# Kernel optimization log

Hardware: AMD Instinct MI355X
Metric: run time of the kernel (lower is better)

## Reference

```python
import jax, jax.numpy as jnp
import numpy as np

H = 16          # num_heads
DH = 128        # head_dim
TILE = 128      # tile_size
TOPK = 8        # top_k_tiles
NEG = -1e10


def _rotate_half(x):
    half = x.shape[-1] // 2
    return jnp.concatenate([-x[..., half:], x[..., :half]], axis=-1)


def setup_inputs() -> dict:
    key = jax.random.key(0)
    B, S, D = 2, 2048, H * DH
    ks = jax.random.split(key, 5)
    x = jax.random.normal(ks[0], (B, S, D), dtype=jnp.float32)
    scale = 0.02
    wq = jax.random.normal(ks[1], (D, H * DH), dtype=jnp.float32) * scale
    wk = jax.random.normal(ks[2], (D, H * DH), dtype=jnp.float32) * scale
    wv = jax.random.normal(ks[3], (D, H * DH), dtype=jnp.float32) * scale
    wo = jax.random.normal(ks[4], (H * DH, D), dtype=jnp.float32) * scale
    # RoPE tables: freqs_cis.real / .imag, shape [S, head_dim//2]
    inv_freq = 1.0 / (10000.0 ** (np.arange(0, DH, 2, dtype=np.float32) / DH))
    angles = np.arange(S, dtype=np.float32)[:, None] * inv_freq[None, :]
    cos = jnp.asarray(np.cos(angles), dtype=jnp.float32)
    sin = jnp.asarray(np.sin(angles), dtype=jnp.float32)
    return {"x": x, "wq": wq, "wk": wk, "wv": wv, "wo": wo, "cos": cos, "sin": sin}


def reference(x, wq, wk, wv, wo, cos, sin):
    B, S, D = x.shape
    # QKV projections -> [B, H, S, Dh]
    q = (x @ wq).reshape(B, S, H, DH).transpose(0, 2, 1, 3)
    k = (x @ wk).reshape(B, S, H, DH).transpose(0, 2, 1, 3)
    v = (x @ wv).reshape(B, S, H, DH).transpose(0, 2, 1, 3)
    # RoPE (half-split / rotate_half form), in fp32 as in source
    cf = jnp.concatenate([cos, cos], axis=-1)[None, None].astype(jnp.float32)  # [1,1,S,Dh]
    sf = jnp.concatenate([sin, sin], axis=-1)[None, None].astype(jnp.float32)
    q = q.astype(jnp.float32)
    k = k.astype(jnp.float32)
    q = q * cf + _rotate_half(q) * sf
    k = k * cf + _rotate_half(k) * sf
    # Full causal logits [B,H,S,S] (short-seq branch: seq_len <= 8192)
    scale = 1.0 / jnp.sqrt(jnp.float32(DH))
    logits = jnp.einsum('bhqd,bhkd->bhqk', q, k) * scale
    causal = jnp.tril(jnp.ones((S, S), dtype=bool))
    logits = jnp.where(causal[None, None], logits, NEG)
    # Tile scoring: softmax over representative rows, tile max-pool, top-k tiles
    num_tiles = S // TILE
    rep_pos = jnp.arange(TILE - 1, S, TILE)           # last query of each tile
    rep_w = jax.nn.softmax(logits[:, :, rep_pos, :], axis=-1)  # [B,H,nt,S]
    tile_scores = jnp.max(rep_w.reshape(B, H, num_tiles, num_tiles, TILE), axis=-1)
    _, group_tile_indices = jax.lax.top_k(tile_scores, min(TOPK, num_tiles))  # [B,H,nt,topk]
    # Full causal attention (explicit path, same math as dot_product_attention is_causal)
    weights = jax.nn.softmax(logits, axis=-1)
    out = jnp.einsum('bhqk,bhkd->bhqd', weights, v)
    out = out.transpose(0, 2, 1, 3).reshape(B, S, H * DH)
    out = out @ wo
    return out, group_tile_indices
```

## Files before the change

### kernel.cpp

```cpp
#include <hip/hip_runtime.h>
#include <cstdint>
#include <cstddef>


#define S_LEN 2048
#define NH 16
#define DHD 128
#define DMODEL 2048
#define MROWS 4096
#define SCALE 0.08838834764831845f
#define SCALE_L2E (0.08838834764831845f * 1.4426950408889634f)
#define NEG10 -1e10f

typedef short short8 __attribute__((ext_vector_type(8)));
typedef __bf16 bf16x8 __attribute__((ext_vector_type(8)));
typedef float f32x4 __attribute__((ext_vector_type(4)));

#define MFMA16(a, b, c) __builtin_amdgcn_mfma_f32_16x16x32_bf16((a), (b), (c), 0, 0, 0)

__device__ __forceinline__ void gl16(const void* g, void* s) {
  __builtin_amdgcn_global_load_lds(
      (const __attribute__((address_space(1))) void*)g,
      (__attribute__((address_space(3))) void*)s, 16, 0, 0);
}

__device__ __forceinline__ unsigned short f2bf(float f) {
  unsigned u = __float_as_uint(f);
  return (unsigned short)((u + 0x7fffu + ((u >> 16) & 1u)) >> 16);
}
__device__ __forceinline__ float bf2f(unsigned short h) {
  return __uint_as_float(((unsigned)h) << 16);
}

__global__ __launch_bounds__(256) void k_split_x(const float* __restrict__ x,
                                                 unsigned short* __restrict__ xh,
                                                 unsigned short* __restrict__ xl, int n4) {
  int i = blockIdx.x * blockDim.x + threadIdx.x;
  for (; i < n4; i += gridDim.x * blockDim.x) {
    float4 v = ((const float4*)x)[i];
    float f[4] = {v.x, v.y, v.z, v.w};
    unsigned short hh[4], ll[4];
#pragma unroll
    for (int j = 0; j < 4; j++) {
      hh[j] = f2bf(f[j]);
      ll[j] = f2bf(f[j] - bf2f(hh[j]));
    }
    ((ushort4*)xh)[i] = make_ushort4(hh[0], hh[1], hh[2], hh[3]);
    ((ushort4*)xl)[i] = make_ushort4(ll[0], ll[1], ll[2], ll[3]);
  }
}

template <int LO>
__global__ __launch_bounds__(256) void k_transw(const float* __restrict__ w,
                                                unsigned short* __restrict__ th,
                                                unsigned short* __restrict__ tl) {
  int n = blockIdx.x * 256 + threadIdx.x;
  int r0 = blockIdx.y * 32;
  float vals[32];
#pragma unroll
  for (int j = 0; j < 32; j++) vals[j] = w[(size_t)(r0 + j) * DMODEL + n];
  unsigned short hs[32];
#pragma unroll
  for (int j = 0; j < 32; j++) hs[j] = f2bf(vals[j]);
  unsigned short* dsth = th + (size_t)n * DMODEL + r0;
#pragma unroll
  for (int c = 0; c < 4; c++) {
    short8 v;
#pragma unroll
    for (int j = 0; j < 8; j++) v[j] = (short)hs[c * 8 + j];
    *(short8*)(dsth + c * 8) = v;
  }
  if (LO) {
    unsigned short ls[32];
#pragma unroll
    for (int j = 0; j < 32; j++) ls[j] = f2bf(vals[j] - bf2f(hs[j]));
    unsigned short* dstl = tl + (size_t)n * DMODEL + r0;
#pragma unroll
    for (int c = 0; c < 4; c++) {
      short8 v;
#pragma unroll
      for (int j = 0; j < 8; j++) v[j] = (short)ls[c * 8 + j];
      *(short8*)(dstl + c * 8) = v;
    }
  }
}

template <int SPLIT, int EPI>
__global__ __launch_bounds__(256) void k_gemm(const unsigned short* __restrict__ A,
                                              const unsigned short* __restrict__ Al,
                                              const unsigned short* __restrict__ Bt,
                                              const unsigned short* __restrict__ Btl,
                                              void* __restrict__ outp) {
  constexpr int NSM = (SPLIT ? 4 : 2) * 4096;
  __shared__ unsigned short sm[NSM];
  unsigned short* sAh = sm;
  unsigned short* sAl = SPLIT ? (sm + 4096) : nullptr;
  unsigned short* sBh = sm + (SPLIT ? 8192 : 4096);
  unsigned short* sBl = SPLIT ? (sm + 12288) : nullptr;

  const int tid = threadIdx.x;
  const int l = tid & 63, w = tid >> 6;
  const int lr = l & 15, lk = l >> 4;
  const int rowBase = blockIdx.y * 128;
  const int colBase = blockIdx.x * 128;
  const int wr = (w >> 1) * 64, wc = (w & 1) * 64;

  f32x4 zero = {0.f, 0.f, 0.f, 0.f};
  f32x4 acc[4][4];
#pragma unroll
  for (int mi = 0; mi < 4; mi++)
#pragma unroll
    for (int ni = 0; ni < 4; ni++) acc[mi][ni] = zero;

  for (int kt = 0; kt < 64; ++kt) {
#pragma unroll
    for (int p = 0; p < 2; ++p) {
      int c = w * 128 + p * 64 + l;
      int row = c >> 2, sl = c & 3;
      int kbl = sl ^ ((row >> 1) & 3);
      size_t srca = (size_t)(rowBase + row) * DMODEL + kt * 32 + kbl * 8;
      gl16(A + srca, (char*)sAh + c * 16);
      if (SPLIT) gl16(Al + srca, (char*)sAl + c * 16);
      size_t srcb = (size_t)(colBase + row) * DMODEL + kt * 32 + kbl * 8;
      gl16(Bt + srcb, (char*)sBh + c * 16);
      if (SPLIT) gl16(Btl + srcb, (char*)sBl + c * 16);
    }
    __syncthreads();

    bf16x8 ah[4], alo[4], bh[4], blo[4];
#pragma unroll
    for (int mi = 0; mi < 4; mi++) {
      int row = wr + mi * 16 + lr;
      int off = row * 32 + ((lk ^ ((row >> 1) & 3)) * 8);
      ah[mi] = *(const bf16x8*)(sAh + off);
      if (SPLIT) alo[mi] = *(const bf16x8*)(sAl + off);
    }
#pragma unroll
    for (int ni = 0; ni < 4; ni++) {
      int row = wc + ni * 16 + lr;
      int off = row * 32 + ((lk ^ ((row >> 1) & 3)) * 8);
      bh[ni] = *(const bf16x8*)(sBh + off);
      if (SPLIT) blo[ni] = *(const bf16x8*)(sBl + off);
    }
#pragma unroll
    for (int mi = 0; mi < 4; mi++)
#pragma unroll
      for (int ni = 0; ni < 4; ni++) {
        acc[mi][ni] = MFMA16(ah[mi], bh[ni], acc[mi][ni]);
        if (SPLIT) {
          acc[mi][ni] = MFMA16(alo[mi], bh[ni], acc[mi][ni]);
          acc[mi][ni] = MFMA16(ah[mi], blo[ni], acc[mi][ni]);
        }
      }
    __syncthreads();
  }

#pragma unroll
  for (int mi = 0; mi < 4; mi++)
#pragma unroll
    for (int ni = 0; ni < 4; ni++)
#pragma unroll
      for (int r = 0; r < 4; r++) {
        int row = rowBase + wr + mi * 16 + lk * 4 + r;
        int col = colBase + wc + ni * 16 + lr;
        float v = acc[mi][ni][r];
        if (EPI == 2) {
          ((float*)outp)[(size_t)row * DMODEL + col] = v;
        } else {
          size_t idx = (((size_t)(row >> 11) * NH + (col >> 7)) * S_LEN + (row & 2047)) * DHD +
                       (col & 127);
          if (EPI == 1)
            ((float*)outp)[idx] = v;
          else
            ((unsigned short*)outp)[idx] = f2bf(v);
        }
      }
}

__global__ __launch_bounds__(256) void k_rope_q(unsigned short* __restrict__ q,
                                                const float* __restrict__ cosT,
                                                const float* __restrict__ sinT) {
  int t = blockIdx.x * blockDim.x + threadIdx.x;
  int row = t >> 4;
  int i4 = (t & 15) * 4;
  int s = row & 2047;
  unsigned short* p0 = q + (size_t)row * DHD + i4;
  unsigned short* p1 = p0 + 64;
  ushort4 a = *(ushort4*)p0, b = *(ushort4*)p1;
  float4 c = *(const float4*)(cosT + (size_t)s * 64 + i4);
  float4 sn = *(const float4*)(sinT + (size_t)s * 64 + i4);
  float av[4] = {bf2f(a.x), bf2f(a.y), bf2f(a.z), bf2f(a.w)};
  float bv[4] = {bf2f(b.x), bf2f(b.y), bf2f(b.z), bf2f(b.w)};
  float cv[4] = {c.x, c.y, c.z, c.w}, sv[4] = {sn.x, sn.y, sn.z, sn.w};
  unsigned short na[4], nb[4];
#pragma unroll
  for (int j = 0; j < 4; j++) {
    na[j] = f2bf(av[j] * cv[j] - bv[j] * sv[j]);
    nb[j] = f2bf(bv[j] * cv[j] + av[j] * sv[j]);
  }
  *(ushort4*)p0 = make_ushort4(na[0], na[1], na[2], na[3]);
  *(ushort4*)p1 = make_ushort4(nb[0], nb[1], nb[2], nb[3]);
}

__global__ __launch_bounds__(256) void k_rope_k(float* __restrict__ kf,
                                                unsigned short* __restrict__ kb,
                                                const float* __restrict__ cosT,
                                                const float* __restrict__ sinT) {
  int t = blockIdx.x * blockDim.x + threadIdx.x;
  int row = t >> 4;
  int i4 = (t & 15) * 4;
  int s = row & 2047;
  float* p0 = kf + (size_t)row * DHD + i4;
  float* p1 = p0 + 64;
  float4 a = *(float4*)p0, b = *(float4*)p1;
  float4 c = *(const float4*)(cosT + (size_t)s * 64 + i4);
  float4 sn = *(const float4*)(sinT + (size_t)s * 64 + i4);
  float av[4] = {a.x, a.y, a.z, a.w}, bv[4] = {b.x, b.y, b.z, b.w};
  float cv[4] = {c.x, c.y, c.z, c.w}, sv[4] = {sn.x, sn.y, sn.z, sn.w};
  float na[4], nb[4];
#pragma unroll
  for (int j = 0; j < 4; j++) {
    na[j] = av[j] * cv[j] - bv[j] * sv[j];
    nb[j] = bv[j] * cv[j] + av[j] * sv[j];
  }
  *(float4*)p0 = make_float4(na[0], na[1], na[2], na[3]);
  *(float4*)p1 = make_float4(nb[0], nb[1], nb[2], nb[3]);
  unsigned short* kb0 = kb + (size_t)row * DHD + i4;
  *(ushort4*)kb0 = make_ushort4(f2bf(na[0]), f2bf(na[1]), f2bf(na[2]), f2bf(na[3]));
  *(ushort4*)(kb0 + 64) = make_ushort4(f2bf(nb[0]), f2bf(nb[1]), f2bf(nb[2]), f2bf(nb[3]));
}

__global__ __launch_bounds__(256) void k_vtrans(const unsigned short* __restrict__ v,
                                                unsigned short* __restrict__ vt) {
  int bh = blockIdx.y;
  int s0 = blockIdx.x * 64 + (threadIdx.x >> 7) * 32;
  int d = threadIdx.x & 127;
  unsigned short tmp[32];
#pragma unroll
  for (int j = 0; j < 32; j++) tmp[j] = v[((size_t)bh * S_LEN + s0 + j) * DHD + d];
  unsigned short* dst = vt + ((size_t)bh * DHD + d) * S_LEN + s0;
#pragma unroll
  for (int c = 0; c < 4; c++) {
    short8 x;
#pragma unroll
    for (int j = 0; j < 8; j++) x[j] = (short)tmp[c * 8 + j];
    *(short8*)(dst + c * 8) = x;
  }
}

__global__ __launch_bounds__(256, 3) void k_attn(const unsigned short* __restrict__ q,
                                                 const unsigned short* __restrict__ k,
                                                 const unsigned short* __restrict__ vt,
                                                 unsigned short* __restrict__ o) {
  __shared__ unsigned short sK[64 * 128];
  __shared__ unsigned short sV[128 * 64];
  __shared__ unsigned short sP[64 * 72];
  const int qt = blockIdx.x, bh = blockIdx.y;
  const int b = bh >> 4, h = bh & 15;
  const int tid = threadIdx.x, l = tid & 63, w = tid >> 6;
  const int lr = l & 15, lk = l >> 4;
  const int q0 = qt * 64;
  const size_t kvbase = (size_t)bh * S_LEN * DHD;

  bf16x8 qf[4];
#pragma unroll
  for (int kd = 0; kd < 4; kd++) {
    int row = q0 + w * 16 + lr;
    qf[kd] = *(const bf16x8*)(q + kvbase + (size_t)row * DHD + kd * 32 + lk * 8);
  }

  f32x4 zero = {0.f, 0.f, 0.f, 0.f};
  f32x4 acc[8];
#pragma unroll
  for (int ni = 0; ni < 8; ni++) acc[ni] = zero;
  float mrow[4], lsum[4];
#pragma unroll
  for (int r = 0; r < 4; r++) {
    mrow[r] = -1e38f;
    lsum[r] = 0.f;
  }

  for (int kt = 0; kt <= qt; ++kt) {
#pragma unroll
    for (int p = 0; p < 4; ++p) {
      int c = p * 256 + tid;
      int kp = c >> 4, sl = c & 15;
      int sls = sl ^ (kp & 7);
      gl16(k + kvbase + (size_t)(kt * 64 + kp) * DHD + sls * 8, (char*)sK + c * 16);
    }
#pragma unroll
    for (int p = 0; p < 4; ++p) {
      int c = p * 256 + tid;
      int dh = c >> 3, sl = c & 7;
      int sls = sl ^ (dh & 7);
      gl16(vt + ((size_t)bh * DHD + dh) * S_LEN + kt * 64 + sls * 8, (char*)sV + c * 16);
    }
    __syncthreads();

    f32x4 sf[4];
#pragma unroll
    for (int nk = 0; nk < 4; nk++) {
      f32x4 sacc = zero;
#pragma unroll
      for (int kd = 0; kd < 4; kd++) {
        int row = nk * 16 + lr;
        int off = row * 128 + (((kd * 4 + lk) ^ (row & 7)) * 8);
        bf16x8 kfrag = *(const bf16x8*)(sK + off);
        sacc = MFMA16(qf[kd], kfrag, sacc);
      }
      sf[nk] = sacc;
    }

    const bool diag = (kt == qt);
#pragma unroll
    for (int r = 0; r < 4; r++) {
      int qpos = q0 + w * 16 + lk * 4 + r;
      float lg[4];
      float mx = -3e38f;
#pragma unroll
      for (int nk = 0; nk < 4; nk++) {
        int kpos = kt * 64 + nk * 16 + lr;
        float vsc = sf[nk][r] * SCALE_L2E;
        if (diag && kpos > qpos) vsc = -3e38f;
        lg[nk] = vsc;
        mx = fmaxf(mx, vsc);
      }
#pragma unroll
      for (int d = 1; d < 16; d <<= 1) mx = fmaxf(mx, __shfl_xor(mx, d));
      float mnew = fmaxf(mrow[r], mx);
      float corr = exp2f(mrow[r] - mnew);
      float ps = 0.f;
      unsigned short pb[4];
#pragma unroll
      for (int nk = 0; nk < 4; nk++) {
        float p = exp2f(lg[nk] - mnew);
        ps += p;
        pb[nk] = f2bf(p);
      }
#pragma unroll
      for (int d = 1; d < 16; d <<= 1) ps += __shfl_xor(ps, d);
      lsum[r] = lsum[r] * corr + ps;
      mrow[r] = mnew;
#pragma unroll
      for (int ni = 0; ni < 8; ni++) acc[ni][r] *= corr;
      int prow = w * 16 + lk * 4 + r;
#pragma unroll
      for (int nk = 0; nk < 4; nk++) sP[prow * 72 + nk * 16 + lr] = pb[nk];
    }
    __syncthreads();

    bf16x8 pa[2];
#pragma unroll
    for (int ks = 0; ks < 2; ks++) {
      int row = w * 16 + lr;
      pa[ks] = *(const bf16x8*)(sP + row * 72 + ks * 32 + lk * 8);
    }
#pragma unroll
    for (int ni = 0; ni < 8; ni++) {
#pragma unroll
      for (int ks = 0; ks < 2; ks++) {
        int row = ni * 16 + lr;
        int off = row * 64 + (((ks * 4 + lk) ^ (row & 7)) * 8);
        bf16x8 vf = *(const bf16x8*)(sV + off);
        acc[ni] = MFMA16(pa[ks], vf, acc[ni]);
      }
    }
    __syncthreads();
  }

#pragma unroll
  for (int r = 0; r < 4; r++) {
    float inv = 1.0f / lsum[r];
    int srow = q0 + w * 16 + lk * 4 + r;
    size_t base = ((size_t)b * S_LEN + srow) * DMODEL + h * DHD;
#pragma unroll
    for (int ni = 0; ni < 8; ni++) o[base + ni * 16 + lr] = f2bf(acc[ni][r] * inv);
  }
}

__global__ __launch_bounds__(256) void k_score(const float* __restrict__ x,
                                               const float* __restrict__ wq,
                                               const float* __restrict__ cosT,
                                               const float* __restrict__ sinT,
                                               const float* __restrict__ kf,
                                               float* __restrict__ idxout) {
  const int t = blockIdx.x, bh = blockIdx.y;
  const int b = bh >> 4, h = bh & 15;
  const int srep = t * 128 + 127;
  const int tid = threadIdx.x;
  __shared__ float qr[128];
  __shared__ float part[256];
  __shared__ unsigned keys[16];

  {
    const int dh = tid & 127, half = tid >> 7;
    const float* xrow = x + ((size_t)b * S_LEN + srep) * DMODEL;
    const float* wcol = wq + (size_t)h * DHD + dh;
    float s0 = 0.f, s1 = 0.f, s2 = 0.f, s3 = 0.f;
    const int dbase = half * 1024;
    for (int d = 0; d < 1024; d += 4) {
      int dd = dbase + d;
      s0 = fmaf(xrow[dd], wcol[(size_t)dd * DMODEL], s0);
      s1 = fmaf(xrow[dd + 1], wcol[(size_t)(dd + 1) * DMODEL], s1);
      s2 = fmaf(xrow[dd + 2], wcol[(size_t)(dd + 2) * DMODEL], s2);
      s3 = fmaf(xrow[dd + 3], wcol[(size_t)(dd + 3) * DMODEL], s3);
    }
    part[tid] = (s0 + s1) + (s2 + s3);
  }
  if (tid < 16) keys[tid] = ~__float_as_uint(NEG10);
  __syncthreads();
  if (tid < 64) {
    int i = tid;
    float q0v = part[i] + part[i + 128];
    float q1v = part[i + 64] + part[i + 192];
    float c = cosT[(size_t)srep * 64 + i], sn = sinT[(size_t)srep * 64 + i];
    qr[i] = q0v * c - q1v * sn;
    qr[i + 64] = q1v * c + q0v * sn;
  }
  __syncthreads();

  for (int j = tid; j <= srep; j += 256) {
    const float4* krow = (const float4*)(kf + ((size_t)bh * S_LEN + j) * DHD);
    float a0 = 0.f, a1 = 0.f, a2 = 0.f, a3 = 0.f;
#pragma unroll 8
    for (int d4 = 0; d4 < 32; d4++) {
      float4 kv = krow[d4];
      const float* qq = qr + d4 * 4;
      a0 = fmaf(kv.x, qq[0], a0);
      a1 = fmaf(kv.y, qq[1], a1);
      a2 = fmaf(kv.z, qq[2], a2);
      a3 = fmaf(kv.w, qq[3], a3);
    }
    float lg = ((a0 + a1) + (a2 + a3)) * SCALE;
    unsigned u = __float_as_uint(lg);
    unsigned key = (u & 0x80000000u) ? ~u : (u | 0x80000000u);
    atomicMax(&keys[j >> 7], key);
  }
  __syncthreads();

  if (tid == 0) {
    unsigned used = 0;
    float* dst = idxout + ((size_t)bh * 16 + t) * 8;
    for (int r = 0; r < 8; ++r) {
      int best = -1;
      unsigned bk = 0;
#pragma unroll
      for (int tl = 0; tl < 16; ++tl) {
        if (used & (1u << tl)) continue;
        unsigned kv = keys[tl];
        if (best < 0 || kv > bk) {
          bk = kv;
          best = tl;
        }
      }
      used |= (1u << best);
      dst[r] = (float)best;
    }
  }
}

extern "C" void kernel_launch(void* const* d_in, const int* in_sizes, int n_in,
                              void* d_out, int out_size, void* d_ws, size_t ws_size,
                              hipStream_t stream) {
  (void)in_sizes; (void)n_in; (void)out_size; (void)ws_size;
  const float* x = (const float*)d_in[0];
  const float* wq = (const float*)d_in[1];
  const float* wk = (const float*)d_in[2];
  const float* wv = (const float*)d_in[3];
  const float* wo = (const float*)d_in[4];
  const float* cosT = (const float*)d_in[5];
  const float* sinT = (const float*)d_in[6];
  float* out0 = (float*)d_out;
  float* out1 = out0 + (size_t)MROWS * DMODEL;
  float* kf32 = out0;

  char* ws = (char*)d_ws;
  size_t off = 0;
  auto alloc = [&](size_t bytes) {
    void* p = ws + off;
    off += (bytes + 255) & ~(size_t)255;
    return p;
  };
  unsigned short* xh = (unsigned short*)alloc(16777216);
  unsigned short* xl = (unsigned short*)alloc(16777216);
  unsigned short* wqT = (unsigned short*)alloc(8388608);
  unsigned short* wkT = (unsigned short*)alloc(8388608);
  unsigned short* wkTl = (unsigned short*)alloc(8388608);
  unsigned short* wvT = (unsigned short*)alloc(8388608);
  unsigned short* woT = (unsigned short*)alloc(8388608);
  unsigned short* qbf = (unsigned short*)alloc(16777216);
  unsigned short* kbf = (unsigned short*)alloc(16777216);
  unsigned short* vbf = (unsigned short*)alloc(16777216);
  unsigned short* obf = xh;
  unsigned short* vtbf = xl;

  k_split_x<<<2048, 256, 0, stream>>>(x, xh, xl, MROWS * DMODEL / 4);
  dim3 gtw(8, 64);
  k_transw<0><<<gtw, 256, 0, stream>>>(wq, wqT, nullptr);
  k_transw<1><<<gtw, 256, 0, stream>>>(wk, wkT, wkTl);
  k_transw<0><<<gtw, 256, 0, stream>>>(wv, wvT, nullptr);
  k_transw<0><<<gtw, 256, 0, stream>>>(wo, woT, nullptr);

  dim3 gg(16, 32);
  k_gemm<0, 0><<<gg, 256, 0, stream>>>(xh, nullptr, wqT, nullptr, qbf);
  k_gemm<1, 1><<<gg, 256, 0, stream>>>(xh, xl, wkT, wkTl, kf32);
  k_gemm<0, 0><<<gg, 256, 0, stream>>>(xh, nullptr, wvT, nullptr, vbf);

  k_rope_q<<<4096, 256, 0, stream>>>(qbf, cosT, sinT);
  k_rope_k<<<4096, 256, 0, stream>>>(kf32, kbf, cosT, sinT);

  k_vtrans<<<dim3(32, 32), 256, 0, stream>>>(vbf, vtbf);
  k_attn<<<dim3(32, 32), 256, 0, stream>>>(qbf, kbf, vtbf, obf);

  k_score<<<dim3(16, 32), 256, 0, stream>>>(x, wq, cosT, sinT, kf32, out1);

  k_gemm<0, 2><<<gg, 256, 0, stream>>>(obf, nullptr, woT, nullptr, out0);
}
```

Baseline: 700.4 us.

## Pair complementary causal query tiles per block to balance attention work

Each attention block now processes two query tiles (p and 31-p) sharing the same K/V tile loads, so every block does an equal amount of causal work and K/V is loaded once for both. The online softmax defers the row-sum shuffle reduction to the end and only rescales when the max increases. Grid is remapped to 512 blocks with an XCD-aware workid swizzle, and occupancy hint drops to 2 blocks per CU, trading more registers and LDS per block for fewer total loads and no tail imbalance.

```diff
diff --git a/kernel.cpp b/kernel.cpp
--- a/kernel.cpp
+++ b/kernel.cpp
@@ -248,133 +248,165 @@
   }
 }
 
-__global__ __launch_bounds__(256, 3) void k_attn(const unsigned short* __restrict__ q,
+__device__ __forceinline__ void attn_qk_sm(const bf16x8 (&qf)[4], f32x4 (&acc)[8],
+                                           float (&mrow)[4], float (&lsum)[4],
+                                           const unsigned short* sK, __bf16* sP,
+                                           int ktbase, bool diag, int q0, int w, int lr,
+                                           int lk) {
+  f32x4 zero = {0.f, 0.f, 0.f, 0.f};
+  f32x4 sf[4];
+#pragma unroll
+  for (int nk = 0; nk < 4; nk++) {
+    f32x4 sacc = zero;
+#pragma unroll
+    for (int kd = 0; kd < 4; kd++) {
+      int row = nk * 16 + lr;
+      int off = row * 128 + (((kd * 4 + lk) ^ (row & 7)) * 8);
+      bf16x8 kfrag = *(const bf16x8*)(sK + off);
+      sacc = MFMA16(qf[kd], kfrag, sacc);
+    }
+    sf[nk] = sacc;
+  }
+#pragma unroll
+  for (int r = 0; r < 4; r++) {
+    int qpos = q0 + w * 16 + lk * 4 + r;
+    float lg[4];
+    float mx = -3e38f;
+#pragma unroll
+    for (int nk = 0; nk < 4; nk++) {
+      int kpos = ktbase + nk * 16 + lr;
+      float vsc = sf[nk][r] * SCALE_L2E;
+      if (diag && kpos > qpos) vsc = -3e38f;
+      lg[nk] = vsc;
+      mx = fmaxf(mx, vsc);
+    }
+#pragma unroll
+    for (int d = 1; d < 16; d <<= 1) mx = fmaxf(mx, __shfl_xor(mx, d));
+    if (mx > mrow[r]) {
+      float corr = exp2f(mrow[r] - mx);
+      mrow[r] = mx;
+      lsum[r] *= corr;
+#pragma unroll
+      for (int ni = 0; ni < 8; ni++) acc[ni][r] *= corr;
+    }
+    float m = mrow[r];
+    float ps = 0.f;
+    int prow = w * 16 + lk * 4 + r;
+#pragma unroll
+    for (int nk = 0; nk < 4; nk++) {
+      float pv = exp2f(lg[nk] - m);
+      ps += pv;
+      sP[prow * 72 + nk * 16 + lr] = (__bf16)pv;
+    }
+    lsum[r] += ps;
+  }
+}
+
+__device__ __forceinline__ void attn_pv(f32x4 (&acc)[8], const __bf16* sP,
+                                        const unsigned short* sV, int w, int lr, int lk) {
+  bf16x8 pa[2];
+#pragma unroll
+  for (int ks = 0; ks < 2; ks++) {
+    int row = w * 16 + lr;
+    pa[ks] = *(const bf16x8*)(sP + row * 72 + ks * 32 + lk * 8);
+  }
+#pragma unroll
+  for (int ni = 0; ni < 8; ni++) {
+#pragma unroll
+    for (int ks = 0; ks < 2; ks++) {
+      int row = ni * 16 + lr;
+      int off = row * 64 + (((ks * 4 + lk) ^ (row & 7)) * 8);
+      bf16x8 vf = *(const bf16x8*)(sV + off);
+      acc[ni] = MFMA16(pa[ks], vf, acc[ni]);
+    }
+  }
+}
+
+__global__ __launch_bounds__(256, 2) void k_attn(const unsigned short* __restrict__ q,
                                                  const unsigned short* __restrict__ k,
                                                  const unsigned short* __restrict__ vt,
                                                  unsigned short* __restrict__ o) {
   __shared__ unsigned short sK[64 * 128];
   __shared__ unsigned short sV[128 * 64];
-  __shared__ unsigned short sP[64 * 72];
-  const int qt = blockIdx.x, bh = blockIdx.y;
+  __shared__ __bf16 sPA[64 * 72];
+  __shared__ __bf16 sPB[64 * 72];
+
+  const int bid = blockIdx.x;
+  const int workid = (bid & 7) * 64 + (bid >> 3);
+  const int bh = workid >> 4, p = workid & 15;
+  const int qtA = p, qtB = 31 - p;
   const int b = bh >> 4, h = bh & 15;
   const int tid = threadIdx.x, l = tid & 63, w = tid >> 6;
   const int lr = l & 15, lk = l >> 4;
-  const int q0 = qt * 64;
+  const int q0A = qtA * 64, q0B = qtB * 64;
   const size_t kvbase = (size_t)bh * S_LEN * DHD;
 
-  bf16x8 qf[4];
+  bf16x8 qfA[4], qfB[4];
 #pragma unroll
   for (int kd = 0; kd < 4; kd++) {
-    int row = q0 + w * 16 + lr;
-    qf[kd] = *(const bf16x8*)(q + kvbase + (size_t)row * DHD + kd * 32 + lk * 8);
+    qfA[kd] = *(const bf16x8*)(q + kvbase + (size_t)(q0A + w * 16 + lr) * DHD + kd * 32 + lk * 8);
+    qfB[kd] = *(const bf16x8*)(q + kvbase + (size_t)(q0B + w * 16 + lr) * DHD + kd * 32 + lk * 8);
   }
 
   f32x4 zero = {0.f, 0.f, 0.f, 0.f};
-  f32x4 acc[8];
-#pragma unroll
-  for (int ni = 0; ni < 8; ni++) acc[ni] = zero;
-  float mrow[4], lsum[4];
+  f32x4 accA[8], accB[8];
+  float mrowA[4], lsumA[4], mrowB[4], lsumB[4];
+#pragma unroll
+  for (int ni = 0; ni < 8; ni++) { accA[ni] = zero; accB[ni] = zero; }
 #pragma unroll
   for (int r = 0; r < 4; r++) {
-    mrow[r] = -1e38f;
-    lsum[r] = 0.f;
-  }
-
-  for (int kt = 0; kt <= qt; ++kt) {
-#pragma unroll
-    for (int p = 0; p < 4; ++p) {
-      int c = p * 256 + tid;
+    mrowA[r] = -3e38f; lsumA[r] = 0.f;
+    mrowB[r] = -3e38f; lsumB[r] = 0.f;
+  }
+
+  for (int kt = 0; kt <= qtB; ++kt) {
+#pragma unroll
+    for (int pp = 0; pp < 4; ++pp) {
+      int c = pp * 256 + tid;
       int kp = c >> 4, sl = c & 15;
       int sls = sl ^ (kp & 7);
       gl16(k + kvbase + (size_t)(kt * 64 + kp) * DHD + sls * 8, (char*)sK + c * 16);
     }
 #pragma unroll
-    for (int p = 0; p < 4; ++p) {
-      int c = p * 256 + tid;
+    for (int pp = 0; pp < 4; ++pp) {
+      int c = pp * 256 + tid;
       int dh = c >> 3, sl = c & 7;
       int sls = sl ^ (dh & 7);
       gl16(vt + ((size_t)bh * DHD + dh) * S_LEN + kt * 64 + sls * 8, (char*)sV + c * 16);
     }
     __syncthreads();
 
-    f32x4 sf[4];
-#pragma unroll
-    for (int nk = 0; nk < 4; nk++) {
-      f32x4 sacc = zero;
-#pragma unroll
-      for (int kd = 0; kd < 4; kd++) {
-        int row = nk * 16 + lr;
-        int off = row * 128 + (((kd * 4 + lk) ^ (row & 7)) * 8);
-        bf16x8 kfrag = *(const bf16x8*)(sK + off);
-        sacc = MFMA16(qf[kd], kfrag, sacc);
-      }
-      sf[nk] = sacc;
-    }
-
-    const bool diag = (kt == qt);
-#pragma unroll
-    for (int r = 0; r < 4; r++) {
-      int qpos = q0 + w * 16 + lk * 4 + r;
-      float lg[4];
-      float mx = -3e38f;
-#pragma unroll
-      for (int nk = 0; nk < 4; nk++) {
-        int kpos = kt * 64 + nk * 16 + lr;
-        float vsc = sf[nk][r] * SCALE_L2E;
-        if (diag && kpos > qpos) vsc = -3e38f;
-        lg[nk] = vsc;
-        mx = fmaxf(mx, vsc);
-      }
-#pragma unroll
-      for (int d = 1; d < 16; d <<= 1) mx = fmaxf(mx, __shfl_xor(mx, d));
-      float mnew = fmaxf(mrow[r], mx);
-      float corr = exp2f(mrow[r] - mnew);
-      float ps = 0.f;
-      unsigned short pb[4];
-#pragma unroll
-      for (int nk = 0; nk < 4; nk++) {
-        float p = exp2f(lg[nk] - mnew);
-        ps += p;
-        pb[nk] = f2bf(p);
-      }
-#pragma unroll
-      for (int d = 1; d < 16; d <<= 1) ps += __shfl_xor(ps, d);
-      lsum[r] = lsum[r] * corr + ps;
-      mrow[r] = mnew;
-#pragma unroll
-      for (int ni = 0; ni < 8; ni++) acc[ni][r] *= corr;
-      int prow = w * 16 + lk * 4 + r;
-#pragma unroll
-      for (int nk = 0; nk < 4; nk++) sP[prow * 72 + nk * 16 + lr] = pb[nk];
-    }
+    const bool doA = (kt <= qtA);
+    attn_qk_sm(qfB, accB, mrowB, lsumB, sK, sPB, kt * 64, kt == qtB, q0B, w, lr, lk);
+    if (doA)
+      attn_qk_sm(qfA, accA, mrowA, lsumA, sK, sPA, kt * 64, kt == qtA, q0A, w, lr, lk);
     __syncthreads();
 
-    bf16x8 pa[2];
-#pragma unroll
-    for (int ks = 0; ks < 2; ks++) {
-      int row = w * 16 + lr;
-      pa[ks] = *(const bf16x8*)(sP + row * 72 + ks * 32 + lk * 8);
-    }
+    attn_pv(accB, sPB, sV, w, lr, lk);
+    if (doA) attn_pv(accA, sPA, sV, w, lr, lk);
+    __syncthreads();
+  }
+
+#pragma unroll
+  for (int r = 0; r < 4; r++) {
+#pragma unroll
+    for (int d = 1; d < 16; d <<= 1) {
+      lsumA[r] += __shfl_xor(lsumA[r], d);
+      lsumB[r] += __shfl_xor(lsumB[r], d);
+    }
+  }
+#pragma unroll
+  for (int r = 0; r < 4; r++) {
+    float invA = 1.0f / lsumA[r], invB = 1.0f / lsumB[r];
+    int srowA = q0A + w * 16 + lk * 4 + r;
+    int srowB = q0B + w * 16 + lk * 4 + r;
+    size_t baseA = ((size_t)b * S_LEN + srowA) * DMODEL + h * DHD;
+    size_t baseB = ((size_t)b * S_LEN + srowB) * DMODEL + h * DHD;
 #pragma unroll
     for (int ni = 0; ni < 8; ni++) {
-#pragma unroll
-      for (int ks = 0; ks < 2; ks++) {
-        int row = ni * 16 + lr;
-        int off = row * 64 + (((ks * 4 + lk) ^ (row & 7)) * 8);
-        bf16x8 vf = *(const bf16x8*)(sV + off);
-        acc[ni] = MFMA16(pa[ks], vf, acc[ni]);
-      }
-    }
-    __syncthreads();
-  }
-
-#pragma unroll
-  for (int r = 0; r < 4; r++) {
-    float inv = 1.0f / lsum[r];
-    int srow = q0 + w * 16 + lk * 4 + r;
-    size_t base = ((size_t)b * S_LEN + srow) * DMODEL + h * DHD;
-#pragma unroll
-    for (int ni = 0; ni < 8; ni++) o[base + ni * 16 + lr] = f2bf(acc[ni][r] * inv);
+      o[baseA + ni * 16 + lr] = f2bf(accA[ni][r] * invA);
+      o[baseB + ni * 16 + lr] = f2bf(accB[ni][r] * invB);
+    }
   }
 }
 
@@ -510,7 +542,7 @@
   k_rope_k<<<4096, 256, 0, stream>>>(kf32, kbf, cosT, sinT);
 
   k_vtrans<<<dim3(32, 32), 256, 0, stream>>>(vbf, vtbf);
-  k_attn<<<dim3(32, 32), 256, 0, stream>>>(qbf, kbf, vtbf, obf);
+  k_attn<<<512, 256, 0, stream>>>(qbf, kbf, vtbf, obf);
 
   k_score<<<dim3(16, 32), 256, 0, stream>>>(x, wq, cosT, sinT, kf32, out1);
 
```

Result: faster. 685.1 us (-2.2%).
